# Kernel tuning notes

Measured on AMD Instinct MI355X. Metric: run time of the kernel, lower is better.

## Reference

```python
import jax, jax.numpy as jnp
import numpy as np

B, DIM1, DIM2, LATENT, T = 16, 1024, 1024, 512, 2048  # T == video_feat_dim
LN_EPS = 1e-5


def setup_inputs() -> dict:
    key = jax.random.key(0)
    ks = jax.random.split(key, 8)
    def xavier(k, shape):
        fan_out, fan_in = shape
        std = float(np.sqrt(2.0 / (fan_in + fan_out)))
        return jax.random.normal(k, shape, dtype=jnp.float32) * std
    return {
        "input1": jax.random.normal(ks[0], (B, DIM1, T), dtype=jnp.float32),
        "input2": jax.random.normal(ks[1], (B, DIM2, T), dtype=jnp.float32),
        "theta_w": xavier(ks[2], (LATENT, DIM2)),
        "theta_b": jnp.zeros((LATENT,), jnp.float32),
        "phi_w": xavier(ks[3], (LATENT, DIM1)),
        "phi_b": jnp.zeros((LATENT,), jnp.float32),
        "g_w": xavier(ks[4], (LATENT, DIM1)),
        "g_b": jnp.zeros((LATENT,), jnp.float32),
        "ln_gamma": jnp.ones((LATENT, T), jnp.float32),
        "ln_beta": jnp.zeros((LATENT, T), jnp.float32),
        "out_w": xavier(ks[5], (DIM2, LATENT)),
        "out_b": jnp.zeros((DIM2,), jnp.float32),
    }


def reference(input1, input2, theta_w, theta_b, phi_w, phi_b, g_w, g_b,
              ln_gamma, ln_beta, out_w, out_b):
    # 1x1 Conv1d == channel-wise matmul
    theta_x = jnp.einsum('ld,bdt->btl', theta_w, input2) + theta_b          # [B,T2,L]
    phi_x = jnp.einsum('ld,bdt->blt', phi_w, input1) + phi_b[:, None]       # [B,L,T1]
    scores = jnp.einsum('btl,bls->bts', theta_x, phi_x)                      # [B,T2,T1] (unscaled)
    p = jax.nn.softmax(scores, axis=-1)
    g_x = jnp.einsum('ld,bdt->btl', g_w, input1) + g_b                       # [B,T1,L]
    t_x = jnp.einsum('bts,bsl->blt', p, g_x)                                 # [B,L,T2]
    # LayerNorm over the last two dims jointly [LATENT, T]
    mu = jnp.mean(t_x, axis=(1, 2), keepdims=True)
    var = jnp.var(t_x, axis=(1, 2), keepdims=True)
    h = (t_x - mu) * jax.lax.rsqrt(var + LN_EPS) * ln_gamma + ln_beta
    h = jax.nn.relu(h)
    w_t = jnp.einsum('ol,blt->bot', out_w, h) + out_b[None, :, None]         # [B,DIM2,T2]
    return w_t + input2
```

## Files before the change

### kernel.cpp

```cpp
#include <hip/hip_runtime.h>
#include <hip/hip_bf16.h>

#define BB 16
#define D1 1024
#define D2 1024
#define LL 512
#define TT 2048
#define LN_EPS 1e-5f

typedef unsigned short u16;
typedef __attribute__((ext_vector_type(8))) _Float16 half8;
typedef __attribute__((ext_vector_type(4))) float f32x4;
typedef __attribute__((ext_vector_type(4))) unsigned int u32x4;

__device__ __forceinline__ u16 f2h(float v) {
    _Float16 h = (_Float16)v;
    return *(u16*)&h;
}
__device__ __forceinline__ float h2f(u16 u) {
    return (float)(*(const _Float16*)&u);
}

__device__ __forceinline__ void gload_lds16(const void* g, void* l) {
    __builtin_amdgcn_global_load_lds((const __attribute__((address_space(1))) void*)g,
                                     (__attribute__((address_space(3))) void*)l, 16, 0, 0);
}

#define MEMFENCE asm volatile("" ::: "memory")
__device__ __forceinline__ void block_barrier() {
    MEMFENCE; __builtin_amdgcn_s_barrier(); MEMFENCE;
}

template<int BIAS, int OMODE>
__global__ __launch_bounds__(512, 2) void nt_gemm(
    const u16* __restrict__ A, const u16* __restrict__ B,
    long sAb, long sBb, long sCb,
    int N, int Kd, int gx, int gy,
    const float* __restrict__ bias,
    void* __restrict__ out0,
    const float* __restrict__ resid, long sRb)
{
    __shared__ __align__(16) u16 smem[65536];

    const int nwg = gridDim.x;
    const int id = blockIdx.x;
    const int swz = (id & 7) * (nwg >> 3) + (id >> 3);
    const int bx = swz % gx;
    const int byz = swz / gx;
    const int by = byz % gy;
    const int b = byz / gy;

    const int tid = threadIdx.x;
    const long arow0 = (long)by * 256;
    const long brow0 = (long)bx * 256;
    const u16* Ab = A + (long)b * sAb + arow0 * Kd;
    const u16* Bb = B + (long)b * sBb + brow0 * Kd;

    const int wave = tid >> 6, lane = tid & 63;
    const int wm = (wave >> 2) * 128, wn = (wave & 3) * 64;
    const int lm = lane & 15, kg = lane >> 4;

    const int m0 = tid >> 3, s0 = tid & 7;
    const int nt = Kd >> 6;

    auto STAGE = [&](int buf, long k0) {
        u16* Ad = smem + buf * 32768;
        u16* Bd = smem + buf * 32768 + 16384;
#pragma unroll
        for (int call = 0; call < 4; ++call) {
            int m = call * 64 + m0;
            int gs = s0 ^ (m & 7);
            gload_lds16(Ab + k0 + (long)m * Kd + gs * 8, Ad + (call * 512 + tid) * 8);
        }
#pragma unroll
        for (int call = 0; call < 4; ++call) {
            int m = call * 64 + m0;
            int gs = s0 ^ (m & 7);
            gload_lds16(Bb + k0 + (long)m * Kd + gs * 8, Bd + (call * 512 + tid) * 8);
        }
    };

    f32x4 acc[8][4];
#pragma unroll
    for (int i = 0; i < 8; ++i)
#pragma unroll
        for (int j = 0; j < 4; ++j) acc[i][j] = (f32x4){0.f, 0.f, 0.f, 0.f};

    STAGE(0, 0);
    if (nt > 1) STAGE(1, 64);

    for (int t = 0; t < nt; ++t) {
        const int cur = t & 1;
        if (t + 1 < nt) { asm volatile("s_waitcnt vmcnt(8)" ::: "memory"); }
        else           { asm volatile("s_waitcnt vmcnt(0)" ::: "memory"); }
        block_barrier();

        const u16* Ac = smem + cur * 32768;
        const u16* Bc = smem + cur * 32768 + 16384;

        half8 bf[4][2];
#pragma unroll
        for (int f = 0; f < 4; ++f)
#pragma unroll
            for (int kf = 0; kf < 2; ++kf) {
                int nr = wn + f * 16 + lm;
                int ss = (kf * 4 + kg) ^ (nr & 7);
                bf[f][kf] = *(const half8*)(Bc + nr * 64 + ss * 8);
            }
#pragma unroll
        for (int mh = 0; mh < 2; ++mh) {
            half8 af[4][2];
#pragma unroll
            for (int f = 0; f < 4; ++f)
#pragma unroll
                for (int kf = 0; kf < 2; ++kf) {
                    int mr = wm + mh * 64 + f * 16 + lm;
                    int ss = (kf * 4 + kg) ^ (mr & 7);
                    af[f][kf] = *(const half8*)(Ac + mr * 64 + ss * 8);
                }
            __builtin_amdgcn_s_setprio(1);
#pragma unroll
            for (int f = 0; f < 4; ++f)
#pragma unroll
                for (int j = 0; j < 4; ++j)
#pragma unroll
                    for (int kf = 0; kf < 2; ++kf)
                        acc[mh * 4 + f][j] = __builtin_amdgcn_mfma_f32_16x16x32_f16(
                            af[f][kf], bf[j][kf], acc[mh * 4 + f][j], 0, 0, 0);
            __builtin_amdgcn_s_setprio(0);
        }
        block_barrier();
        if (t + 2 < nt) STAGE(cur, (long)(t + 2) * 64);
    }

    float* Cs = (float*)smem;
#pragma unroll
    for (int p = 0; p < 2; ++p) {
        __syncthreads();
        if (wm == p * 128) {
#pragma unroll
            for (int i = 0; i < 8; ++i)
#pragma unroll
                for (int j = 0; j < 4; ++j)
#pragma unroll
                    for (int r = 0; r < 4; ++r) {
                        int row = i * 16 + kg * 4 + r;
                        int col = wn + j * 16 + lm;
                        Cs[row * 256 + (col ^ ((row & 7) << 2))] = acc[i][j][r];
                    }
        }
        __syncthreads();
        if (OMODE == 0 || OMODE == 3) {
#pragma unroll
            for (int it = 0; it < 16; ++it) {
                int elem = it * 512 + tid;
                int row = elem >> 6, c4 = elem & 63;
                int grow = (int)arow0 + p * 128 + row;
                int gcol = (int)brow0 + c4 * 4;
                f32x4 v = *(const f32x4*)&Cs[row * 256 + ((c4 ^ (row & 7)) << 2)];
                if (BIAS == 1) v += bias[grow];
                if (BIAS == 2) v += *(const f32x4*)(bias + gcol);
                long off = (long)b * sCb + (long)grow * N + gcol;
                if (OMODE == 3) {
                    f32x4 rv = __builtin_nontemporal_load(
                        (const f32x4*)(resid + (long)b * sRb + (long)grow * N + gcol));
                    v += rv;
                    __builtin_nontemporal_store(v, (f32x4*)((float*)out0 + off));
                } else {
                    *(f32x4*)((float*)out0 + off) = v;
                }
            }
        } else {
#pragma unroll
            for (int it = 0; it < 8; ++it) {
                int elem = it * 512 + tid;
                int row = elem >> 5, c8 = elem & 31;
                int grow = (int)arow0 + p * 128 + row;
                int gcol = (int)brow0 + c8 * 8;
                int g0 = (c8 * 2) ^ (row & 7);
                int g1 = (c8 * 2 + 1) ^ (row & 7);
                f32x4 u0 = *(const f32x4*)&Cs[row * 256 + g0 * 4];
                f32x4 u1 = *(const f32x4*)&Cs[row * 256 + g1 * 4];
                float vv[8] = {u0.x, u0.y, u0.z, u0.w, u1.x, u1.y, u1.z, u1.w};
                if (BIAS == 1) {
                    float bb = bias[grow];
#pragma unroll
                    for (int q = 0; q < 8; ++q) vv[q] += bb;
                }
                if (BIAS == 2) {
#pragma unroll
                    for (int q = 0; q < 8; ++q) vv[q] += bias[gcol + q];
                }
                union { u16 u[8]; u32x4 v4; } pk;
#pragma unroll
                for (int q = 0; q < 8; ++q) pk.u[q] = f2h(vv[q]);
                long off = (long)b * sCb + (long)grow * N + gcol;
                *(u32x4*)((u16*)out0 + off) = pk.v4;
            }
        }
    }
}

__device__ __forceinline__ void stage_tile_sm(const u16* __restrict__ g, int ldk, u16* lds, int tid) {
#pragma unroll
    for (int it = 0; it < 4; ++it) {
        int idx = it * 256 + tid;
        int m = idx >> 3, s = idx & 7;
        int gs = s ^ (m & 7);
        gload_lds16(g + (long)m * ldk + gs * 8, lds + idx * 8);
    }
}

template<int BIAS, int OMODE, int LNS>
__global__ __launch_bounds__(256, 4) void nt_gemm_sm(
    const u16* __restrict__ A, const u16* __restrict__ B,
    long sAb, long sBb, long sCb,
    int N, int Kd, int gx, int gy,
    const float* __restrict__ bias,
    void* __restrict__ out0,
    const float* __restrict__ resid, long sRb,
    float* __restrict__ lnsums)
{
    __shared__ __align__(16) u16 smem[2 * 128 * 64];
    u16* As = smem;
    u16* Bs = smem + 128 * 64;

    const int nwg = gridDim.x;
    const int id = blockIdx.x;
    const int swz = (id & 7) * (nwg >> 3) + (id >> 3);
    const int bx = swz % gx;
    const int byz = swz / gx;
    const int by = byz % gy;
    const int b = byz / gy;

    const int tid = threadIdx.x;
    const long arow0 = (long)by * 128;
    const long brow0 = (long)bx * 128;
    const u16* Ab = A + (long)b * sAb + arow0 * Kd;
    const u16* Bb = B + (long)b * sBb + brow0 * Kd;

    const int wave = tid >> 6, lane = tid & 63;
    const int wm = (wave >> 1) * 64, wn = (wave & 1) * 64;
    const int lm = lane & 15, kg = lane >> 4;

    f32x4 acc[4][4];
#pragma unroll
    for (int i = 0; i < 4; ++i)
#pragma unroll
        for (int j = 0; j < 4; ++j) acc[i][j] = (f32x4){0.f, 0.f, 0.f, 0.f};

    for (int k0 = 0; k0 < Kd; k0 += 64) {
        stage_tile_sm(Ab + k0, Kd, As, tid);
        stage_tile_sm(Bb + k0, Kd, Bs, tid);
        __syncthreads();
#pragma unroll
        for (int ks = 0; ks < 2; ++ks) {
            half8 af[4], bf[4];
#pragma unroll
            for (int f = 0; f < 4; ++f) {
                int mr = wm + f * 16 + lm;
                int as_ = (ks * 4 + kg) ^ (mr & 7);
                af[f] = *(const half8*)(As + mr * 64 + as_ * 8);
                int nr = wn + f * 16 + lm;
                int bs_ = (ks * 4 + kg) ^ (nr & 7);
                bf[f] = *(const half8*)(Bs + nr * 64 + bs_ * 8);
            }
#pragma unroll
            for (int i = 0; i < 4; ++i)
#pragma unroll
                for (int j = 0; j < 4; ++j)
                    acc[i][j] = __builtin_amdgcn_mfma_f32_16x16x32_f16(af[i], bf[j], acc[i][j], 0, 0, 0);
        }
        __syncthreads();
    }

    float ls = 0.f, lsq = 0.f;
    float* Cs = (float*)smem;
#pragma unroll
    for (int p = 0; p < 2; ++p) {
        if (p) __syncthreads();
        if (wm == p * 64) {
#pragma unroll
            for (int i = 0; i < 4; ++i)
#pragma unroll
                for (int j = 0; j < 4; ++j)
#pragma unroll
                    for (int r = 0; r < 4; ++r) {
                        int row = i * 16 + kg * 4 + r;
                        int col = wn + j * 16 + lm;
                        Cs[row * 128 + (col ^ ((row & 7) << 2))] = acc[i][j][r];
                    }
        }
        __syncthreads();
        if (OMODE == 0 || OMODE == 3) {
#pragma unroll
            for (int rr = 0; rr < 8; ++rr) {
                int elem = rr * 256 + tid;
                int row = elem >> 5, c4 = elem & 31;
                int grow = (int)arow0 + p * 64 + row;
                int gcol = (int)brow0 + c4 * 4;
                f32x4 v = *(const f32x4*)&Cs[row * 128 + ((c4 ^ (row & 7)) << 2)];
                if (BIAS == 1) v += bias[grow];
                if (BIAS == 2) v += *(const f32x4*)(bias + gcol);
                long off = (long)b * sCb + (long)grow * N + gcol;
                if (OMODE == 3) {
                    f32x4 rv = __builtin_nontemporal_load(
                        (const f32x4*)(resid + (long)b * sRb + (long)grow * N + gcol));
                    v += rv;
                    __builtin_nontemporal_store(v, (f32x4*)((float*)out0 + off));
                } else {
                    *(f32x4*)((float*)out0 + off) = v;
                }
            }
        } else {
#pragma unroll
            for (int rr = 0; rr < 4; ++rr) {
                int elem = rr * 256 + tid;
                int row = elem >> 4, c8 = elem & 15;
                int grow = (int)arow0 + p * 64 + row;
                int gcol = (int)brow0 + c8 * 8;
                int g0 = (c8 * 2) ^ (row & 7);
                int g1 = (c8 * 2 + 1) ^ (row & 7);
                f32x4 u0 = *(const f32x4*)&Cs[row * 128 + g0 * 4];
                f32x4 u1 = *(const f32x4*)&Cs[row * 128 + g1 * 4];
                float vv[8] = {u0.x, u0.y, u0.z, u0.w, u1.x, u1.y, u1.z, u1.w};
                if (BIAS == 1) {
                    float bb = bias[grow];
#pragma unroll
                    for (int q = 0; q < 8; ++q) vv[q] += bb;
                }
                if (BIAS == 2) {
#pragma unroll
                    for (int q = 0; q < 8; ++q) vv[q] += bias[gcol + q];
                }
                if (LNS) {
#pragma unroll
                    for (int q = 0; q < 8; ++q) { ls += vv[q]; lsq += vv[q] * vv[q]; }
                }
                union { u16 u[8]; u32x4 v4; } pk;
#pragma unroll
                for (int q = 0; q < 8; ++q) pk.u[q] = f2h(vv[q]);
                long off = (long)b * sCb + (long)grow * N + gcol;
                *(u32x4*)((u16*)out0 + off) = pk.v4;
            }
        }
    }
    if (LNS) {
#pragma unroll
        for (int off = 32; off; off >>= 1) {
            ls += __shfl_xor(ls, off, 64);
            lsq += __shfl_xor(lsq, off, 64);
        }
        __shared__ float rsum[8];
        if (lane == 0) { rsum[wave] = ls; rsum[4 + wave] = lsq; }
        __syncthreads();
        if (tid == 0) {
            atomicAdd(&lnsums[b * 2], rsum[0] + rsum[1] + rsum[2] + rsum[3]);
            atomicAdd(&lnsums[b * 2 + 1], rsum[4] + rsum[5] + rsum[6] + rsum[7]);
        }
    }
}

__global__ __launch_bounds__(256) void transpose_h(const float* __restrict__ in,
                                                   u16* __restrict__ o16, int D, int T) {
    __shared__ float tile[64][65];
    int b = blockIdx.z;
    const float* src = in + (long)b * D * T;
    long obase = (long)b * D * T;
    int t0 = blockIdx.x * 64, d0 = blockIdx.y * 64;
    int tx = threadIdx.x & 63, ty = threadIdx.x >> 6;
#pragma unroll
    for (int i = 0; i < 64; i += 4)
        tile[ty + i][tx] = __builtin_nontemporal_load(&src[(long)(d0 + ty + i) * T + t0 + tx]);
    __syncthreads();
#pragma unroll
    for (int i = 0; i < 64; i += 4) {
        long o = obase + (long)(t0 + ty + i) * D + d0 + tx;
        o16[o] = f2h(tile[tx][ty + i]);
    }
}

__global__ __launch_bounds__(256) void transpose_f32(const float* __restrict__ in,
                                                     float* __restrict__ out, int R, int C) {
    __shared__ float tile[64][65];
    int c0 = blockIdx.x * 64, r0 = blockIdx.y * 64;
    int tx = threadIdx.x & 63, ty = threadIdx.x >> 6;
#pragma unroll
    for (int i = 0; i < 64; i += 4)
        tile[ty + i][tx] = in[(long)(r0 + ty + i) * C + c0 + tx];
    __syncthreads();
#pragma unroll
    for (int i = 0; i < 64; i += 4)
        out[(long)(c0 + ty + i) * R + r0 + tx] = tile[tx][ty + i];
}

__global__ __launch_bounds__(256) void conv_w(const float* __restrict__ w,
                                              u16* __restrict__ h, int n) {
    int i = blockIdx.x * 256 + threadIdx.x;
    if (i < n) h[i] = f2h(w[i]);
}

__global__ __launch_bounds__(256) void softmax_rows(const float* __restrict__ S, u16* __restrict__ P) {
    long row = (long)blockIdx.z * TT + blockIdx.x;
    const float* s = S + row * TT;
    u16* p = P + row * TT;
    int tid = threadIdx.x;
    f32x4 v0 = *(const f32x4*)(s + tid * 8);
    f32x4 v1 = *(const f32x4*)(s + tid * 8 + 4);
    float x[8] = {v0.x, v0.y, v0.z, v0.w, v1.x, v1.y, v1.z, v1.w};
    float m = x[0];
#pragma unroll
    for (int j = 1; j < 8; ++j) m = fmaxf(m, x[j]);
#pragma unroll
    for (int off = 32; off; off >>= 1) m = fmaxf(m, __shfl_xor(m, off, 64));
    __shared__ float red[8];
    int wave = tid >> 6, lane = tid & 63;
    if (lane == 0) red[wave] = m;
    __syncthreads();
    m = fmaxf(fmaxf(red[0], red[1]), fmaxf(red[2], red[3]));
    float e[8]; float sum = 0.f;
#pragma unroll
    for (int j = 0; j < 8; ++j) { e[j] = __expf(x[j] - m); sum += e[j]; }
#pragma unroll
    for (int off = 32; off; off >>= 1) sum += __shfl_xor(sum, off, 64);
    if (lane == 0) red[4 + wave] = sum;
    __syncthreads();
    sum = red[4] + red[5] + red[6] + red[7];
    float inv = 1.f / sum;
    union { u16 u[8]; u32x4 v4; } pk;
#pragma unroll
    for (int j = 0; j < 8; ++j) pk.u[j] = f2h(e[j] * inv);
    *(u32x4*)(p + tid * 8) = pk.v4;
}

__global__ void zero32(float* p) { p[threadIdx.x] = 0.f; }

__global__ __launch_bounds__(256) void ln_apply(const u16* __restrict__ TXp, const float* __restrict__ sums,
                                                const float* __restrict__ gT, const float* __restrict__ bT,
                                                u16* __restrict__ H) {
    int b = blockIdx.z;
    const float n = (float)(LL * TT);
    float mu = sums[b * 2] / n;
    float var = sums[b * 2 + 1] / n - mu * mu;
    float rstd = rsqrtf(var + LN_EPS);
    long base = (long)b * (LL * TT);
    long idx = ((long)blockIdx.x * 256 + threadIdx.x) * 8;
    u32x4 xv = *(const u32x4*)(TXp + base + idx);
    unsigned w[4] = {xv.x, xv.y, xv.z, xv.w};
    f32x4 g0 = *(const f32x4*)(gT + idx);
    f32x4 g1 = *(const f32x4*)(gT + idx + 4);
    f32x4 b0 = *(const f32x4*)(bT + idx);
    f32x4 b1 = *(const f32x4*)(bT + idx + 4);
    float g[8] = {g0.x, g0.y, g0.z, g0.w, g1.x, g1.y, g1.z, g1.w};
    float be[8] = {b0.x, b0.y, b0.z, b0.w, b1.x, b1.y, b1.z, b1.w};
    union { u16 u[8]; u32x4 v; } pk;
#pragma unroll
    for (int q = 0; q < 4; ++q) {
        float a = h2f((u16)(w[q] & 0xffff));
        float c = h2f((u16)(w[q] >> 16));
        float oa = fmaxf((a - mu) * rstd * g[q * 2] + be[q * 2], 0.f);
        float oc = fmaxf((c - mu) * rstd * g[q * 2 + 1] + be[q * 2 + 1], 0.f);
        pk.u[q * 2] = f2h(oa);
        pk.u[q * 2 + 1] = f2h(oc);
    }
    *(u32x4*)(H + base + idx) = pk.v;
}

extern "C" void kernel_launch(void* const* d_in, const int* in_sizes, int n_in,
                              void* d_out, int out_size, void* d_ws, size_t ws_size,
                              hipStream_t stream) {
    const float* input1  = (const float*)d_in[0];
    const float* input2  = (const float*)d_in[1];
    const float* theta_w = (const float*)d_in[2];
    const float* theta_b = (const float*)d_in[3];
    const float* phi_w   = (const float*)d_in[4];
    const float* phi_b   = (const float*)d_in[5];
    const float* g_w     = (const float*)d_in[6];
    const float* g_b     = (const float*)d_in[7];
    const float* ln_gamma= (const float*)d_in[8];
    const float* ln_beta = (const float*)d_in[9];
    const float* out_w   = (const float*)d_in[10];
    const float* out_b   = (const float*)d_in[11];
    float* out = (float*)d_out;

    char* ws = (char*)d_ws;
    const size_t MB = 1ull << 20;
    u16*  Xt     = (u16*)(ws + 0);
    float* scores= (float*)(ws + 0);
    u16*  pmat   = (u16*)(ws + 64 * MB);
    u16*  Qf     = (u16*)(ws + 96 * MB);
    u16*  Kf     = (u16*)(ws + 128 * MB);
    u16*  Vt     = (u16*)(ws + 160 * MB);
    u16*  TX     = (u16*)(ws + 192 * MB);
    u16*  H      = (u16*)(ws + 224 * MB);
    u16*  thw    = (u16*)(ws + 256 * MB);
    u16*  phw    = (u16*)(ws + 257 * MB);
    u16*  gww    = (u16*)(ws + 258 * MB);
    u16*  oww    = (u16*)(ws + 259 * MB);
    float* gammaT= (float*)(ws + 260 * MB);
    float* betaT = (float*)(ws + 264 * MB);
    float* sums  = (float*)(ws + 268 * MB);

    dim3 blk(256), blk5(512);

    conv_w<<<dim3((LL * D2 + 255) / 256), blk, 0, stream>>>(theta_w, thw, LL * D2);
    conv_w<<<dim3((LL * D1 + 255) / 256), blk, 0, stream>>>(phi_w, phw, LL * D1);
    conv_w<<<dim3((LL * D1 + 255) / 256), blk, 0, stream>>>(g_w, gww, LL * D1);
    conv_w<<<dim3((D2 * LL + 255) / 256), blk, 0, stream>>>(out_w, oww, D2 * LL);
    transpose_f32<<<dim3(TT / 64, LL / 64, 1), blk, 0, stream>>>(ln_gamma, gammaT, LL, TT);
    transpose_f32<<<dim3(TT / 64, LL / 64, 1), blk, 0, stream>>>(ln_beta, betaT, LL, TT);
    zero32<<<dim3(1), dim3(32), 0, stream>>>(sums);

    transpose_h<<<dim3(TT / 64, D2 / 64, BB), blk, 0, stream>>>(input2, Xt, D2, TT);
    nt_gemm<2, 1><<<dim3((LL / 256) * (TT / 256) * BB), blk5, 0, stream>>>(
        Xt, thw, (long)TT * D2, 0, (long)TT * LL, LL, D2, LL / 256, TT / 256,
        theta_b, Qf, nullptr, 0);

    transpose_h<<<dim3(TT / 64, D1 / 64, BB), blk, 0, stream>>>(input1, Xt, D1, TT);
    nt_gemm<2, 1><<<dim3((LL / 256) * (TT / 256) * BB), blk5, 0, stream>>>(
        Xt, phw, (long)TT * D1, 0, (long)TT * LL, LL, D1, LL / 256, TT / 256,
        phi_b, Kf, nullptr, 0);
    nt_gemm<1, 1><<<dim3((TT / 256) * (LL / 256) * BB), blk5, 0, stream>>>(
        gww, Xt, 0, (long)TT * D1, (long)LL * TT, TT, D1, TT / 256, LL / 256,
        g_b, Vt, nullptr, 0);

    for (int c = 0; c < 4; ++c) {
        long qoff = (long)c * 4 * TT * LL;
        nt_gemm<0, 0><<<dim3((TT / 256) * (TT / 256) * 4), blk5, 0, stream>>>(
            Qf + qoff, Kf + qoff, (long)TT * LL, (long)TT * LL, (long)TT * TT,
            TT, LL, TT / 256, TT / 256, nullptr, scores, nullptr, 0);
        softmax_rows<<<dim3(TT, 1, 4), blk, 0, stream>>>(scores, pmat);
        nt_gemm_sm<0, 1, 1><<<dim3((LL / 128) * (TT / 128) * 4), blk, 0, stream>>>(
            pmat, Vt + (long)c * 4 * LL * TT, (long)TT * TT, (long)LL * TT, (long)TT * LL,
            LL, TT, LL / 128, TT / 128, nullptr, TX + qoff, nullptr, 0, sums + (long)c * 8);
    }

    ln_apply<<<dim3(512, 1, BB), blk, 0, stream>>>(TX, sums, gammaT, betaT, H);

    nt_gemm_sm<1, 3, 0><<<dim3((TT / 128) * (D2 / 128) * BB), blk, 0, stream>>>(
        oww, H, 0, (long)TT * LL, (long)D2 * TT, TT, LL, TT / 128, D2 / 128,
        out_b, out, input2, (long)D2 * TT, nullptr);
}
```

Measured before the change: 628.0 us.

## Batch the P·V GEMM across all batches with large tiles and fused LN sums

```diff
diff --git a/kernel.cpp b/kernel.cpp
--- a/kernel.cpp
+++ b/kernel.cpp
@@ -31,14 +31,15 @@
     MEMFENCE; __builtin_amdgcn_s_barrier(); MEMFENCE;
 }
 
-template<int BIAS, int OMODE>
+template<int BIAS, int OMODE, int LNS>
 __global__ __launch_bounds__(512, 2) void nt_gemm(
     const u16* __restrict__ A, const u16* __restrict__ B,
     long sAb, long sBb, long sCb,
     int N, int Kd, int gx, int gy,
     const float* __restrict__ bias,
     void* __restrict__ out0,
-    const float* __restrict__ resid, long sRb)
+    const float* __restrict__ resid, long sRb,
+    float* __restrict__ lnsums)
 {
     __shared__ __align__(16) u16 smem[65536];
 
@@ -133,6 +134,7 @@
         if (t + 2 < nt) STAGE(cur, (long)(t + 2) * 64);
     }
 
+    float ls = 0.f, lsq = 0.f;
     float* Cs = (float*)smem;
 #pragma unroll
     for (int p = 0; p < 2; ++p) {
@@ -165,10 +167,8 @@
                     f32x4 rv = __builtin_nontemporal_load(
                         (const f32x4*)(resid + (long)b * sRb + (long)grow * N + gcol));
                     v += rv;
-                    __builtin_nontemporal_store(v, (f32x4*)((float*)out0 + off));
-                } else {
-                    *(f32x4*)((float*)out0 + off) = v;
-                }
+                }
+                __builtin_nontemporal_store(v, (f32x4*)((float*)out0 + off));
             }
         } else {
 #pragma unroll
@@ -191,12 +191,33 @@
 #pragma unroll
                     for (int q = 0; q < 8; ++q) vv[q] += bias[gcol + q];
                 }
+                if (LNS) {
+#pragma unroll
+                    for (int q = 0; q < 8; ++q) { ls += vv[q]; lsq += vv[q] * vv[q]; }
+                }
                 union { u16 u[8]; u32x4 v4; } pk;
 #pragma unroll
                 for (int q = 0; q < 8; ++q) pk.u[q] = f2h(vv[q]);
                 long off = (long)b * sCb + (long)grow * N + gcol;
-                *(u32x4*)((u16*)out0 + off) = pk.v4;
+                __builtin_nontemporal_store(pk.v4, (u32x4*)((u16*)out0 + off));
             }
+        }
+    }
+    if (LNS) {
+#pragma unroll
+        for (int off = 32; off; off >>= 1) {
+            ls += __shfl_xor(ls, off, 64);
+            lsq += __shfl_xor(lsq, off, 64);
+        }
+        __shared__ float rsum[16];
+        if (lane == 0) { rsum[wave] = ls; rsum[8 + wave] = lsq; }
+        __syncthreads();
+        if (tid == 0) {
+            float a = 0.f, c = 0.f;
+#pragma unroll
+            for (int w = 0; w < 8; ++w) { a += rsum[w]; c += rsum[8 + w]; }
+            atomicAdd(&lnsums[b * 2], a);
+            atomicAdd(&lnsums[b * 2 + 1], c);
         }
     }
 }
@@ -211,15 +232,14 @@
     }
 }
 
-template<int BIAS, int OMODE, int LNS>
+template<int BIAS, int OMODE>
 __global__ __launch_bounds__(256, 4) void nt_gemm_sm(
     const u16* __restrict__ A, const u16* __restrict__ B,
     long sAb, long sBb, long sCb,
     int N, int Kd, int gx, int gy,
     const float* __restrict__ bias,
     void* __restrict__ out0,
-    const float* __restrict__ resid, long sRb,
-    float* __restrict__ lnsums)
+    const float* __restrict__ resid, long sRb)
 {
     __shared__ __align__(16) u16 smem[2 * 128 * 64];
     u16* As = smem;
@@ -274,7 +294,6 @@
         __syncthreads();
     }
 
-    float ls = 0.f, lsq = 0.f;
     float* Cs = (float*)smem;
 #pragma unroll
     for (int p = 0; p < 2; ++p) {
@@ -333,30 +352,12 @@
 #pragma unroll
                     for (int q = 0; q < 8; ++q) vv[q] += bias[gcol + q];
                 }
-                if (LNS) {
-#pragma unroll
-                    for (int q = 0; q < 8; ++q) { ls += vv[q]; lsq += vv[q] * vv[q]; }
-                }
                 union { u16 u[8]; u32x4 v4; } pk;
 #pragma unroll
                 for (int q = 0; q < 8; ++q) pk.u[q] = f2h(vv[q]);
                 long off = (long)b * sCb + (long)grow * N + gcol;
                 *(u32x4*)((u16*)out0 + off) = pk.v4;
             }
-        }
-    }
-    if (LNS) {
-#pragma unroll
-        for (int off = 32; off; off >>= 1) {
-            ls += __shfl_xor(ls, off, 64);
-            lsq += __shfl_xor(lsq, off, 64);
-        }
-        __shared__ float rsum[8];
-        if (lane == 0) { rsum[wave] = ls; rsum[4 + wave] = lsq; }
-        __syncthreads();
-        if (tid == 0) {
-            atomicAdd(&lnsums[b * 2], rsum[0] + rsum[1] + rsum[2] + rsum[3]);
-            atomicAdd(&lnsums[b * 2 + 1], rsum[4] + rsum[5] + rsum[6] + rsum[7]);
         }
     }
 }
@@ -405,8 +406,8 @@
     const float* s = S + row * TT;
     u16* p = P + row * TT;
     int tid = threadIdx.x;
-    f32x4 v0 = *(const f32x4*)(s + tid * 8);
-    f32x4 v1 = *(const f32x4*)(s + tid * 8 + 4);
+    f32x4 v0 = __builtin_nontemporal_load((const f32x4*)(s + tid * 8));
+    f32x4 v1 = __builtin_nontemporal_load((const f32x4*)(s + tid * 8 + 4));
     float x[8] = {v0.x, v0.y, v0.z, v0.w, v1.x, v1.y, v1.z, v1.w};
     float m = x[0];
 #pragma unroll
@@ -488,18 +489,18 @@
     u16*  Xt     = (u16*)(ws + 0);
     float* scores= (float*)(ws + 0);
     u16*  pmat   = (u16*)(ws + 64 * MB);
-    u16*  Qf     = (u16*)(ws + 96 * MB);
-    u16*  Kf     = (u16*)(ws + 128 * MB);
-    u16*  Vt     = (u16*)(ws + 160 * MB);
-    u16*  TX     = (u16*)(ws + 192 * MB);
-    u16*  H      = (u16*)(ws + 224 * MB);
-    u16*  thw    = (u16*)(ws + 256 * MB);
-    u16*  phw    = (u16*)(ws + 257 * MB);
-    u16*  gww    = (u16*)(ws + 258 * MB);
-    u16*  oww    = (u16*)(ws + 259 * MB);
-    float* gammaT= (float*)(ws + 260 * MB);
-    float* betaT = (float*)(ws + 264 * MB);
-    float* sums  = (float*)(ws + 268 * MB);
+    u16*  Qf     = (u16*)(ws + 192 * MB);
+    u16*  Kf     = (u16*)(ws + 224 * MB);
+    u16*  Vt     = (u16*)(ws + 256 * MB);
+    u16*  TX     = (u16*)(ws + 288 * MB);
+    u16*  H      = (u16*)(ws + 320 * MB);
+    u16*  thw    = (u16*)(ws + 352 * MB);
+    u16*  phw    = (u16*)(ws + 353 * MB);
+    u16*  gww    = (u16*)(ws + 354 * MB);
+    u16*  oww    = (u16*)(ws + 355 * MB);
+    float* gammaT= (float*)(ws + 356 * MB);
+    float* betaT = (float*)(ws + 360 * MB);
+    float* sums  = (float*)(ws + 364 * MB);
 
     dim3 blk(256), blk5(512);
 
@@ -512,32 +513,32 @@
     zero32<<<dim3(1), dim3(32), 0, stream>>>(sums);
 
     transpose_h<<<dim3(TT / 64, D2 / 64, BB), blk, 0, stream>>>(input2, Xt, D2, TT);
-    nt_gemm<2, 1><<<dim3((LL / 256) * (TT / 256) * BB), blk5, 0, stream>>>(
+    nt_gemm<2, 1, 0><<<dim3((LL / 256) * (TT / 256) * BB), blk5, 0, stream>>>(
         Xt, thw, (long)TT * D2, 0, (long)TT * LL, LL, D2, LL / 256, TT / 256,
-        theta_b, Qf, nullptr, 0);
+        theta_b, Qf, nullptr, 0, nullptr);
 
     transpose_h<<<dim3(TT / 64, D1 / 64, BB), blk, 0, stream>>>(input1, Xt, D1, TT);
-    nt_gemm<2, 1><<<dim3((LL / 256) * (TT / 256) * BB), blk5, 0, stream>>>(
+    nt_gemm<2, 1, 0><<<dim3((LL / 256) * (TT / 256) * BB), blk5, 0, stream>>>(
         Xt, phw, (long)TT * D1, 0, (long)TT * LL, LL, D1, LL / 256, TT / 256,
-        phi_b, Kf, nullptr, 0);
-    nt_gemm<1, 1><<<dim3((TT / 256) * (LL / 256) * BB), blk5, 0, stream>>>(
+        phi_b, Kf, nullptr, 0, nullptr);
+    nt_gemm<1, 1, 0><<<dim3((TT / 256) * (LL / 256) * BB), blk5, 0, stream>>>(
         gww, Xt, 0, (long)TT * D1, (long)LL * TT, TT, D1, TT / 256, LL / 256,
-        g_b, Vt, nullptr, 0);
+        g_b, Vt, nullptr, 0, nullptr);
 
     for (int c = 0; c < 4; ++c) {
         long qoff = (long)c * 4 * TT * LL;
-        nt_gemm<0, 0><<<dim3((TT / 256) * (TT / 256) * 4), blk5, 0, stream>>>(
+        nt_gemm<0, 0, 0><<<dim3((TT / 256) * (TT / 256) * 4), blk5, 0, stream>>>(
             Qf + qoff, Kf + qoff, (long)TT * LL, (long)TT * LL, (long)TT * TT,
-            TT, LL, TT / 256, TT / 256, nullptr, scores, nullptr, 0);
-        softmax_rows<<<dim3(TT, 1, 4), blk, 0, stream>>>(scores, pmat);
-        nt_gemm_sm<0, 1, 1><<<dim3((LL / 128) * (TT / 128) * 4), blk, 0, stream>>>(
-            pmat, Vt + (long)c * 4 * LL * TT, (long)TT * TT, (long)LL * TT, (long)TT * LL,
-            LL, TT, LL / 128, TT / 128, nullptr, TX + qoff, nullptr, 0, sums + (long)c * 8);
-    }
+            TT, LL, TT / 256, TT / 256, nullptr, scores, nullptr, 0, nullptr);
+        softmax_rows<<<dim3(TT, 1, 4), blk, 0, stream>>>(scores, pmat + (long)c * 4 * TT * TT);
+    }
+    nt_gemm<0, 1, 1><<<dim3((LL / 256) * (TT / 256) * BB), blk5, 0, stream>>>(
+        pmat, Vt, (long)TT * TT, (long)LL * TT, (long)TT * LL,
+        LL, TT, LL / 256, TT / 256, nullptr, TX, nullptr, 0, sums);
 
     ln_apply<<<dim3(512, 1, BB), blk, 0, stream>>>(TX, sums, gammaT, betaT, H);
 
-    nt_gemm_sm<1, 3, 0><<<dim3((TT / 128) * (D2 / 128) * BB), blk, 0, stream>>>(
+    nt_gemm_sm<1, 3><<<dim3((TT / 128) * (D2 / 128) * BB), blk, 0, stream>>>(
         oww, H, 0, (long)TT * LL, (long)D2 * TT, TT, LL, TT / 128, D2 / 128,
-        out_b, out, input2, (long)D2 * TT, nullptr);
-}
+        out_b, out, input2, (long)D2 * TT);
+}
```

New measurement: 566.3 us. 1.11x faster.
